# Kernel optimization log

Hardware: AMD Instinct MI355X
Metric: run time of the kernel (lower is better)

The kernel has to match this reference:

```python
import jax, jax.numpy as jnp
import numpy as np

N, D, K = 500000, 128, 2048

def setup_inputs() -> dict:
    key = jax.random.key(0)
    kx, kp = jax.random.split(key)
    x = jax.random.normal(kx, (N, D), dtype=jnp.float32)
    p = jax.random.normal(kp, (D,), dtype=jnp.float32)
    return {"x": x, "p": p, "k": K}

def reference(x, p, k):
    # y = x @ p / ||p||  -> [N]
    y = (x @ p) / jnp.linalg.norm(p)
    top_vals, top_idx = jax.lax.top_k(y, k)          # [k], [k]
    # gather top-k rows and scale by tanh of their scores
    out = x[top_idx] * jnp.tanh(top_vals)[:, None]   # [k, D]
    return out
```

## Files before the change

kernel.cpp:

```cpp
#include <hip/hip_runtime.h>
#include <hip/hip_bf16.h>


#define HIST_BITS 12
#define HIST_BINS (1 << HIST_BITS)
#define HIST_SHIFT (32 - HIST_BITS)
#define SORTN 8192

__device__ __forceinline__ unsigned mono_key(float f) {
    unsigned u = __float_as_uint(f);
    return (u & 0x80000000u) ? ~u : (u | 0x80000000u);
}
__device__ __forceinline__ float mono_key_inv(unsigned mk) {
    unsigned u = (mk & 0x80000000u) ? (mk ^ 0x80000000u) : ~mk;
    return __uint_as_float(u);
}

__global__ void score_kernel(const float* __restrict__ x, const float* __restrict__ p,
                             float* __restrict__ y, int N, int rpw) {
    int lane = threadIdx.x & 63;
    int half = lane >> 5;
    int l32  = lane & 31;
    long long gwave = ((long long)blockIdx.x * blockDim.x + threadIdx.x) >> 6;
    long long start = gwave * rpw;
    if (start >= N) return;

    float4 pq = ((const float4*)p)[l32];
    double pp = (double)pq.x * pq.x + (double)pq.y * pq.y +
                (double)pq.z * pq.z + (double)pq.w * pq.w;
    #pragma unroll
    for (int off = 16; off > 0; off >>= 1) pp += __shfl_xor(pp, off, 64);
    double rinv = 1.0 / sqrt(pp);

    long long rend = start + rpw; if (rend > N) rend = N;
    for (long long r0 = start; r0 < rend; r0 += 2) {
        long long row = r0 + half;
        bool valid = row < N;
        float4 xq = valid ? ((const float4*)(x + row * 128))[l32]
                          : make_float4(0.f, 0.f, 0.f, 0.f);
        double d = (double)xq.x * pq.x + (double)xq.y * pq.y +
                   (double)xq.z * pq.z + (double)xq.w * pq.w;
        #pragma unroll
        for (int off = 16; off > 0; off >>= 1) d += __shfl_xor(d, off, 64);
        if (l32 == 0 && valid) y[row] = (float)(d * rinv);
    }
}

__global__ void hist_kernel(const float* __restrict__ y, unsigned* __restrict__ hist, int N) {
    __shared__ unsigned h[4][HIST_BINS];
    for (int i = threadIdx.x; i < 4 * HIST_BINS; i += blockDim.x) h[0][i] = 0;
    __syncthreads();
    int sub = (threadIdx.x >> 6) & 3;
    int stride = gridDim.x * blockDim.x;
    for (int i = blockIdx.x * blockDim.x + threadIdx.x; i < N; i += stride)
        atomicAdd(&h[sub][mono_key(y[i]) >> HIST_SHIFT], 1u);
    __syncthreads();
    for (int i = threadIdx.x; i < HIST_BINS; i += blockDim.x) {
        unsigned v = h[0][i] + h[1][i] + h[2][i] + h[3][i];
        if (v) atomicAdd(&hist[i], v);
    }
}

__global__ void threshold_kernel(const unsigned* __restrict__ hist,
                                 const int* __restrict__ kptr, int* __restrict__ res) {
    __shared__ unsigned s[HIST_BINS];
    int t = threadIdx.x;
    for (int i = t; i < HIST_BINS; i += 1024) s[i] = hist[i];
    __syncthreads();
    for (int off = 1; off < HIST_BINS; off <<= 1) {
        unsigned v[HIST_BINS / 1024];
        #pragma unroll
        for (int j = 0; j < HIST_BINS / 1024; j++) {
            int i = t + j * 1024;
            v[j] = s[i] + ((i + off < HIST_BINS) ? s[i + off] : 0u);
        }
        __syncthreads();
        #pragma unroll
        for (int j = 0; j < HIST_BINS / 1024; j++) s[t + j * 1024] = v[j];
        __syncthreads();
    }
    int k = *kptr;
    #pragma unroll
    for (int j = 0; j < HIST_BINS / 1024; j++) {
        int i = t + j * 1024;
        int c     = (int)s[i];
        int cnext = (i + 1 < HIST_BINS) ? (int)s[i + 1] : 0;
        if (c >= k && cnext < k) { res[0] = i; res[1] = cnext; }
    }
}

__global__ void compact_kernel(const float* __restrict__ y, const int* __restrict__ res,
                               unsigned long long* __restrict__ pairs, int* __restrict__ cnt,
                               int N) {
    __shared__ int lcnt, lbase;
    if (threadIdx.x == 0) lcnt = 0;
    __syncthreads();
    int B = res[0];
    int i = blockIdx.x * blockDim.x + threadIdx.x;
    int lpos = -1;
    unsigned mk = 0;
    if (i < N) {
        mk = mono_key(y[i]);
        if ((int)(mk >> HIST_SHIFT) >= B) lpos = atomicAdd(&lcnt, 1);
    }
    __syncthreads();
    if (threadIdx.x == 0 && lcnt > 0) lbase = atomicAdd(cnt, lcnt);
    __syncthreads();
    if (lpos >= 0) {
        int pos = lbase + lpos;
        if (pos < SORTN)
            pairs[pos] = ((unsigned long long)mk << 32) | (unsigned)~(unsigned)i;
    }
}

__global__ void rank_kernel(const unsigned long long* __restrict__ pairs,
                            const int* __restrict__ cnt,
                            unsigned long long* __restrict__ spairs, int K) {
    __shared__ unsigned long long s[SORTN];
    int n = *cnt; if (n > SORTN) n = SORTN;
    int npad = (n + 3) & ~3;
    for (int i = threadIdx.x; i < npad; i += blockDim.x)
        s[i] = (i < n) ? pairs[i] : 0ull;
    __syncthreads();
    int c = blockIdx.x * blockDim.x + threadIdx.x;
    if (c >= n) return;
    unsigned long long my = s[c];
    int r = 0;
    for (int i = 0; i < npad; i += 4) {
        unsigned long long a = s[i], b = s[i + 1], d = s[i + 2], e = s[i + 3];
        r += (a > my) + (b > my) + (d > my) + (e > my);
    }
    if (r < K) spairs[r] = my;
}

__global__ void gather_kernel(const float* __restrict__ x,
                              const unsigned long long* __restrict__ spairs,
                              float* __restrict__ out) {
    int j = blockIdx.x;
    unsigned long long key = spairs[j];
    unsigned mk  = (unsigned)(key >> 32);
    unsigned idx = ~(unsigned)(key & 0xFFFFFFFFull);
    float scale = tanhf(mono_key_inv(mk));
    int t = threadIdx.x;
    out[(size_t)j * 128 + t] = x[(size_t)idx * 128 + t] * scale;
}

extern "C" void kernel_launch(void* const* d_in, const int* in_sizes, int n_in,
                              void* d_out, int out_size, void* d_ws, size_t ws_size,
                              hipStream_t stream) {
    const float* x = (const float*)d_in[0];
    const float* p = (const float*)d_in[1];
    const int*   kptr = (const int*)d_in[2];
    float* out = (float*)d_out;

    const int D = in_sizes[1];
    const int N = in_sizes[0] / D;
    const int K = out_size / D;
    (void)n_in; (void)ws_size;

    unsigned char* w = (unsigned char*)d_ws;
    float* y = (float*)w;
    size_t off = ((size_t)N * sizeof(float) + 255) & ~(size_t)255;
    unsigned* hist = (unsigned*)(w + off);
    int* cnt = (int*)(w + off + HIST_BINS * sizeof(unsigned));
    int* res = cnt + 1;
    size_t off2 = (off + HIST_BINS * sizeof(unsigned) + 3 * sizeof(int) + 255) & ~(size_t)255;
    unsigned long long* pairs = (unsigned long long*)(w + off2);
    unsigned long long* spairs = pairs + SORTN;

    hipMemsetAsync(hist, 0, HIST_BINS * sizeof(unsigned) + sizeof(int), stream);

    {
        const int blocks = 2048;
        long long total_waves = (long long)blocks * 256 / 64;
        int rpw = (int)((N + total_waves - 1) / total_waves);
        rpw = (rpw + 1) & ~1;
        score_kernel<<<blocks, 256, 0, stream>>>(x, p, y, N, rpw);
    }
    hist_kernel<<<64, 1024, 0, stream>>>(y, hist, N);
    threshold_kernel<<<1, 1024, 0, stream>>>(hist, kptr, res);
    compact_kernel<<<(N + 255) / 256, 256, 0, stream>>>(y, res, pairs, cnt, N);
    rank_kernel<<<SORTN / 256, 256, 0, stream>>>(pairs, cnt, spairs, K);
    gather_kernel<<<K, 128, 0, stream>>>(x, spairs, out);
}
```

Before: 422.9 us.

## Split rank counting across slices and unroll score loop two rows per half-wave

```diff
diff --git a/kernel.cpp b/kernel.cpp
--- a/kernel.cpp
+++ b/kernel.cpp
@@ -6,6 +6,7 @@
 #define HIST_BINS (1 << HIST_BITS)
 #define HIST_SHIFT (32 - HIST_BITS)
 #define SORTN 8192
+#define SLICES 8
 
 __device__ __forceinline__ unsigned mono_key(float f) {
     unsigned u = __float_as_uint(f);
@@ -33,16 +34,26 @@
     double rinv = 1.0 / sqrt(pp);
 
     long long rend = start + rpw; if (rend > N) rend = N;
-    for (long long r0 = start; r0 < rend; r0 += 2) {
-        long long row = r0 + half;
-        bool valid = row < N;
-        float4 xq = valid ? ((const float4*)(x + row * 128))[l32]
-                          : make_float4(0.f, 0.f, 0.f, 0.f);
-        double d = (double)xq.x * pq.x + (double)xq.y * pq.y +
-                   (double)xq.z * pq.z + (double)xq.w * pq.w;
+    for (long long r0 = start; r0 < rend; r0 += 4) {
+        long long rowA = r0 + half;
+        long long rowB = r0 + 2 + half;
+        bool vb = (r0 + 2) < rend;
+        float4 xa = ((const float4*)(x + rowA * 128))[l32];
+        float4 xb = vb ? ((const float4*)(x + rowB * 128))[l32]
+                       : make_float4(0.f, 0.f, 0.f, 0.f);
+        double dA = (double)xa.x * pq.x + (double)xa.y * pq.y +
+                    (double)xa.z * pq.z + (double)xa.w * pq.w;
+        double dB = (double)xb.x * pq.x + (double)xb.y * pq.y +
+                    (double)xb.z * pq.z + (double)xb.w * pq.w;
         #pragma unroll
-        for (int off = 16; off > 0; off >>= 1) d += __shfl_xor(d, off, 64);
-        if (l32 == 0 && valid) y[row] = (float)(d * rinv);
+        for (int off = 16; off > 0; off >>= 1) {
+            dA += __shfl_xor(dA, off, 64);
+            dB += __shfl_xor(dB, off, 64);
+        }
+        if (l32 == 0) {
+            y[rowA] = (float)(dA * rinv);
+            if (vb) y[rowB] = (float)(dB * rinv);
+        }
     }
 }
 
@@ -113,24 +124,40 @@
     }
 }
 
-__global__ void rank_kernel(const unsigned long long* __restrict__ pairs,
-                            const int* __restrict__ cnt,
-                            unsigned long long* __restrict__ spairs, int K) {
-    __shared__ unsigned long long s[SORTN];
+__global__ void rank_count_kernel(const unsigned long long* __restrict__ pairs,
+                                  const int* __restrict__ cnt,
+                                  int* __restrict__ rankpart) {
+    __shared__ unsigned long long s[SORTN / SLICES];
     int n = *cnt; if (n > SORTN) n = SORTN;
-    int npad = (n + 3) & ~3;
-    for (int i = threadIdx.x; i < npad; i += blockDim.x)
-        s[i] = (i < n) ? pairs[i] : 0ull;
+    if ((int)(blockIdx.x * blockDim.x) >= n) return;
+    int npad = (n + 4 * SLICES - 1) & ~(4 * SLICES - 1);
+    int slen = npad / SLICES;
+    int sbeg = blockIdx.y * slen;
+    for (int i = threadIdx.x; i < slen; i += blockDim.x) {
+        int gi = sbeg + i;
+        s[i] = (gi < n) ? pairs[gi] : 0ull;
+    }
     __syncthreads();
     int c = blockIdx.x * blockDim.x + threadIdx.x;
     if (c >= n) return;
-    unsigned long long my = s[c];
+    unsigned long long my = pairs[c];
     int r = 0;
-    for (int i = 0; i < npad; i += 4) {
-        unsigned long long a = s[i], b = s[i + 1], d = s[i + 2], e = s[i + 3];
-        r += (a > my) + (b > my) + (d > my) + (e > my);
-    }
-    if (r < K) spairs[r] = my;
+    for (int i = 0; i < slen; i += 4)
+        r += (int)(s[i] > my) + (int)(s[i+1] > my) + (int)(s[i+2] > my) + (int)(s[i+3] > my);
+    rankpart[blockIdx.y * SORTN + c] = r;
+}
+
+__global__ void rank_scatter_kernel(const unsigned long long* __restrict__ pairs,
+                                    const int* __restrict__ cnt,
+                                    const int* __restrict__ rankpart,
+                                    unsigned long long* __restrict__ spairs, int K) {
+    int n = *cnt; if (n > SORTN) n = SORTN;
+    int c = blockIdx.x * blockDim.x + threadIdx.x;
+    if (c >= n) return;
+    int r = 0;
+    #pragma unroll
+    for (int sl = 0; sl < SLICES; sl++) r += rankpart[sl * SORTN + c];
+    if (r < K) spairs[r] = pairs[c];
 }
 
 __global__ void gather_kernel(const float* __restrict__ x,
@@ -167,6 +194,7 @@
     size_t off2 = (off + HIST_BINS * sizeof(unsigned) + 3 * sizeof(int) + 255) & ~(size_t)255;
     unsigned long long* pairs = (unsigned long long*)(w + off2);
     unsigned long long* spairs = pairs + SORTN;
+    int* rankpart = (int*)(spairs + SORTN);
 
     hipMemsetAsync(hist, 0, HIST_BINS * sizeof(unsigned) + sizeof(int), stream);
 
@@ -180,6 +208,7 @@
     hist_kernel<<<64, 1024, 0, stream>>>(y, hist, N);
     threshold_kernel<<<1, 1024, 0, stream>>>(hist, kptr, res);
     compact_kernel<<<(N + 255) / 256, 256, 0, stream>>>(y, res, pairs, cnt, N);
-    rank_kernel<<<SORTN / 256, 256, 0, stream>>>(pairs, cnt, spairs, K);
+    rank_count_kernel<<<dim3(SORTN / 256, SLICES), 256, 0, stream>>>(pairs, cnt, rankpart);
+    rank_scatter_kernel<<<SORTN / 256, 256, 0, stream>>>(pairs, cnt, rankpart, spairs, K);
     gather_kernel<<<K, 128, 0, stream>>>(x, spairs, out);
 }
```

After: 397.0 us. 1.07x faster.
